# Performance work log

Measured on AMD Instinct MI355X. Metric: run time of the kernel, lower is better.

Reference implementation:

```python
import jax, jax.numpy as jnp
import numpy as np


def setup_inputs() -> dict:
    key = jax.random.key(0)
    k1, k2, k3 = jax.random.split(key, 3)
    # q: [num_seqs, num_heads, head_dim] decode queries (q_len = 1)
    q = jax.random.normal(k1, (32, 32, 128), dtype=jnp.float32)
    # k, v: [sp_shards, num_seqs, kv_len_per_shard, num_kv_heads, head_dim]
    k = jax.random.normal(k2, (4, 32, 1024, 8, 128), dtype=jnp.float32)
    v = jax.random.normal(k3, (4, 32, 1024, 8, 128), dtype=jnp.float32)
    return {"q": q, "k": k, "v": v}


def reference(q, k, v):
    # Flash-decoding style paged decode attention with GQA:
    # each sequence-parallel shard s produces a partial (normalized) output
    # plus per-(seq, head) max logit and exp-sum; gatherlayer then performs
    # the online-softmax merge across shards.
    n, h, d = q.shape
    s, _, L, kv, _ = k.shape
    g = h // kv  # GQA group size
    scale = jnp.asarray(d, q.dtype) ** -0.5
    q4 = q.reshape(n, kv, g, d)

    # --- per-shard partial attention (what self.attn returns per rank) ---
    scores = jnp.einsum('nkgd,snlkd->snkgl', q4, k) * scale  # [s,n,kv,g,L]
    max_logits = scores.max(axis=-1)                          # [s,n,kv,g]
    p = jnp.exp(scores - max_logits[..., None])
    exp_sum = p.sum(axis=-1)                                  # [s,n,kv,g]
    partial = jnp.einsum('snkgl,snlkd->snkgd', p, v) / exp_sum[..., None]

    # --- gatherlayer: online-softmax combine across shards ---
    gmax = max_logits.max(axis=0)                             # [n,kv,g]
    w = jnp.exp(max_logits - gmax) * exp_sum                  # [s,n,kv,g]
    out = (partial * w[..., None]).sum(axis=0) / w.sum(axis=0)[..., None]
    return out.reshape(n, h, d)
```

## Files before the change

kernel.cpp:

```cpp
#include <hip/hip_runtime.h>
#include <math.h>

#define NSEQ 32
#define NH   32
#define NKV  8
#define GRP  4
#define DIM  128
#define NSH  4
#define LSH  1024
#define ITERS 128
#define KVSTRIDE (NKV*DIM)

#define MOFF ((size_t)NSH*NSEQ*NKV*GRP*DIM)
#define SOFF (MOFF + (size_t)NSH*NSEQ*NKV*GRP)

__global__ __launch_bounds__(256, 4) void attn_partial_kernel(
    const float* __restrict__ q, const float* __restrict__ kk,
    const float* __restrict__ vv, float* __restrict__ ws) {
  const int kvh = blockIdx.x;
  const int n   = blockIdx.y;
  const int sh  = blockIdx.z;
  const int tid = threadIdx.x;
  const int w    = tid >> 6;
  const int lane = tid & 63;
  const int sub  = lane & 31;
  const int pgrp = (w << 1) | (lane >> 5);

  const float scale = 0.08838834764831845f;
  const float* qp = q + ((size_t)n * NH + (size_t)kvh * GRP) * DIM + sub * 4;
  float4 qv0 = *(const float4*)(qp + 0 * DIM);
  float4 qv1 = *(const float4*)(qp + 1 * DIM);
  float4 qv2 = *(const float4*)(qp + 2 * DIM);
  float4 qv3 = *(const float4*)(qp + 3 * DIM);
#define SCQ(Q) Q.x *= scale; Q.y *= scale; Q.z *= scale; Q.w *= scale
  SCQ(qv0); SCQ(qv1); SCQ(qv2); SCQ(qv3);
#undef SCQ

  float m0 = -1e30f, m1 = -1e30f, m2 = -1e30f, m3 = -1e30f;
  float s0 = 0.f, s1 = 0.f, s2 = 0.f, s3 = 0.f;
  float4 a0 = make_float4(0.f,0.f,0.f,0.f);
  float4 a1 = a0, a2 = a0, a3 = a0;

  const size_t blkoff = ((size_t)sh * NSEQ + n) * LSH * (size_t)KVSTRIDE
                        + (size_t)kvh * DIM + sub * 4;
  const float* kb = kk + blkoff;
  const float* vb = vv + blkoff;

  auto process = [&](const float4 kc, const float4 vc) {
    float d0 = kc.x*qv0.x + kc.y*qv0.y + kc.z*qv0.z + kc.w*qv0.w;
    float d1 = kc.x*qv1.x + kc.y*qv1.y + kc.z*qv1.z + kc.w*qv1.w;
    float d2 = kc.x*qv2.x + kc.y*qv2.y + kc.z*qv2.z + kc.w*qv2.w;
    float d3 = kc.x*qv3.x + kc.y*qv3.y + kc.z*qv3.z + kc.w*qv3.w;
#pragma unroll
    for (int off = 1; off < 32; off <<= 1) {
      d0 += __shfl_xor(d0, off, 32);
      d1 += __shfl_xor(d1, off, 32);
      d2 += __shfl_xor(d2, off, 32);
      d3 += __shfl_xor(d3, off, 32);
    }
    if (d0 > m0 || d1 > m1 || d2 > m2 || d3 > m3) {
      float nm0 = fmaxf(m0, d0), nm1 = fmaxf(m1, d1);
      float nm2 = fmaxf(m2, d2), nm3 = fmaxf(m3, d3);
      float r0 = __expf(m0 - nm0), r1 = __expf(m1 - nm1);
      float r2 = __expf(m2 - nm2), r3 = __expf(m3 - nm3);
      s0 *= r0; s1 *= r1; s2 *= r2; s3 *= r3;
      a0.x *= r0; a0.y *= r0; a0.z *= r0; a0.w *= r0;
      a1.x *= r1; a1.y *= r1; a1.z *= r1; a1.w *= r1;
      a2.x *= r2; a2.y *= r2; a2.z *= r2; a2.w *= r2;
      a3.x *= r3; a3.y *= r3; a3.z *= r3; a3.w *= r3;
      m0 = nm0; m1 = nm1; m2 = nm2; m3 = nm3;
    }
    float p0 = __expf(d0 - m0), p1 = __expf(d1 - m1);
    float p2 = __expf(d2 - m2), p3 = __expf(d3 - m3);
    s0 += p0; s1 += p1; s2 += p2; s3 += p3;
    a0.x = fmaf(p0, vc.x, a0.x); a0.y = fmaf(p0, vc.y, a0.y);
    a0.z = fmaf(p0, vc.z, a0.z); a0.w = fmaf(p0, vc.w, a0.w);
    a1.x = fmaf(p1, vc.x, a1.x); a1.y = fmaf(p1, vc.y, a1.y);
    a1.z = fmaf(p1, vc.z, a1.z); a1.w = fmaf(p1, vc.w, a1.w);
    a2.x = fmaf(p2, vc.x, a2.x); a2.y = fmaf(p2, vc.y, a2.y);
    a2.z = fmaf(p2, vc.z, a2.z); a2.w = fmaf(p2, vc.w, a2.w);
    a3.x = fmaf(p3, vc.x, a3.x); a3.y = fmaf(p3, vc.y, a3.y);
    a3.z = fmaf(p3, vc.z, a3.z); a3.w = fmaf(p3, vc.w, a3.w);
  };

  float4 k0 = *(const float4*)(kb + (size_t)(0 * 8 + pgrp) * KVSTRIDE);
  float4 v0 = *(const float4*)(vb + (size_t)(0 * 8 + pgrp) * KVSTRIDE);
  float4 k1 = *(const float4*)(kb + (size_t)(1 * 8 + pgrp) * KVSTRIDE);
  float4 v1 = *(const float4*)(vb + (size_t)(1 * 8 + pgrp) * KVSTRIDE);

  for (int it = 0; it < ITERS; it += 2) {
    const int p2i = (it + 2) & (ITERS - 1);
    const int p3i = (it + 3) & (ITERS - 1);
    float4 nk0 = *(const float4*)(kb + (size_t)(p2i * 8 + pgrp) * KVSTRIDE);
    float4 nv0 = *(const float4*)(vb + (size_t)(p2i * 8 + pgrp) * KVSTRIDE);
    float4 nk1 = *(const float4*)(kb + (size_t)(p3i * 8 + pgrp) * KVSTRIDE);
    float4 nv1 = *(const float4*)(vb + (size_t)(p3i * 8 + pgrp) * KVSTRIDE);
    process(k0, v0);
    process(k1, v1);
    k0 = nk0; v0 = nv0; k1 = nk1; v1 = nv1;
  }

#define HALF_MERGE(mX, sX, aX) do {                       \
    float om_ = __shfl_xor(mX, 32, 64);                   \
    float nm_ = fmaxf(mX, om_);                           \
    float ea_ = __expf(mX - nm_), eb_ = __expf(om_ - nm_);\
    float os_ = __shfl_xor(sX, 32, 64);                   \
    sX = sX * ea_ + os_ * eb_;                            \
    float t_;                                             \
    t_ = __shfl_xor(aX.x, 32, 64); aX.x = aX.x*ea_ + t_*eb_; \
    t_ = __shfl_xor(aX.y, 32, 64); aX.y = aX.y*ea_ + t_*eb_; \
    t_ = __shfl_xor(aX.z, 32, 64); aX.z = aX.z*ea_ + t_*eb_; \
    t_ = __shfl_xor(aX.w, 32, 64); aX.w = aX.w*ea_ + t_*eb_; \
    mX = nm_;                                             \
  } while (0)
  HALF_MERGE(m0, s0, a0);
  HALF_MERGE(m1, s1, a1);
  HALF_MERGE(m2, s2, a2);
  HALF_MERGE(m3, s3, a3);
#undef HALF_MERGE

  __shared__ float lm[4][GRP][32];
  __shared__ float lsum[4][GRP][32];
  __shared__ float la[4][GRP][32][4];
  if ((lane >> 5) == 0) {
#define STORE_G(gi, mX, sX, aX)                                   \
    lm[w][gi][sub] = mX; lsum[w][gi][sub] = sX;                   \
    la[w][gi][sub][0] = aX.x; la[w][gi][sub][1] = aX.y;           \
    la[w][gi][sub][2] = aX.z; la[w][gi][sub][3] = aX.w;
    STORE_G(0, m0, s0, a0)
    STORE_G(1, m1, s1, a1)
    STORE_G(2, m2, s2, a2)
    STORE_G(3, m3, s3, a3)
#undef STORE_G
  }
  __syncthreads();

  if (tid < 128) {
    const int gi = tid >> 5;
    const int sb = tid & 31;
    float M = -1e30f, SS = 0.f;
    float A0 = 0.f, A1 = 0.f, A2 = 0.f, A3 = 0.f;
#pragma unroll
    for (int wv = 0; wv < 4; ++wv) {
      float mm = lm[wv][gi][sb];
      float nm = fmaxf(M, mm);
      float ra = __expf(M - nm), rb = __expf(mm - nm);
      SS = SS * ra + lsum[wv][gi][sb] * rb;
      A0 = A0 * ra + la[wv][gi][sb][0] * rb;
      A1 = A1 * ra + la[wv][gi][sb][1] * rb;
      A2 = A2 * ra + la[wv][gi][sb][2] * rb;
      A3 = A3 * ra + la[wv][gi][sb][3] * rb;
      M = nm;
    }
    const size_t idx = (((size_t)sh * NSEQ + n) * NKV + kvh) * GRP + gi;
    *(float4*)(ws + idx * DIM + sb * 4) = make_float4(A0, A1, A2, A3);
    ws[MOFF + idx] = M;
    ws[SOFF + idx] = SS;
  }
}

__global__ __launch_bounds__(128) void attn_merge_kernel(
    const float* __restrict__ ws, float* __restrict__ out) {
  const int kvh = blockIdx.x;
  const int n   = blockIdx.y;
  const int d   = threadIdx.x;
#pragma unroll
  for (int gi = 0; gi < GRP; ++gi) {
    size_t idx[NSH];
    float mm[NSH];
    float M = -1e30f;
#pragma unroll
    for (int s2 = 0; s2 < NSH; ++s2) {
      idx[s2] = (((size_t)s2 * NSEQ + n) * NKV + kvh) * GRP + gi;
      mm[s2] = ws[MOFF + idx[s2]];
      M = fmaxf(M, mm[s2]);
    }
    float num = 0.f, den = 0.f;
#pragma unroll
    for (int s2 = 0; s2 < NSH; ++s2) {
      float wg = __expf(mm[s2] - M);
      den += wg * ws[SOFF + idx[s2]];
      num += wg * ws[idx[s2] * DIM + d];
    }
    out[((size_t)n * NH + (size_t)kvh * GRP + gi) * DIM + d] = num / den;
  }
}

extern "C" void kernel_launch(void* const* d_in, const int* in_sizes, int n_in,
                              void* d_out, int out_size, void* d_ws, size_t ws_size,
                              hipStream_t stream) {
  const float* q = (const float*)d_in[0];
  const float* k = (const float*)d_in[1];
  const float* v = (const float*)d_in[2];
  float* out = (float*)d_out;
  float* ws  = (float*)d_ws;

  attn_partial_kernel<<<dim3(NKV, NSEQ, NSH), 256, 0, stream>>>(q, k, v, ws);
  attn_merge_kernel<<<dim3(NKV, NSEQ), 128, 0, stream>>>(ws, out);
}
```

Before: 185.0 us.

## Fuse cross-shard merge into partial kernel via last-block atomic counter

Removes the separate merge kernel launch. Each partial block increments a per-(kv head, seq) atomic counter, and the last of the four shard blocks to finish performs the online-softmax merge and writes the output. K/V loads now use nontemporal loads, and the prefetch loop drops the wrapped redundant final loads by peeling the last two iterations. In exchange it adds a memset launch for the counters plus threadfence/atomic overhead.

After: 236.9 us. 1.28x slower.

```diff
diff --git a/kernel.cpp b/kernel.cpp
--- a/kernel.cpp
+++ b/kernel.cpp
@@ -13,10 +13,18 @@
 
 #define MOFF ((size_t)NSH*NSEQ*NKV*GRP*DIM)
 #define SOFF (MOFF + (size_t)NSH*NSEQ*NKV*GRP)
-
-__global__ __launch_bounds__(256, 4) void attn_partial_kernel(
+#define CNT_OFF (SOFF + (size_t)NSH*NSEQ*NKV*GRP)
+
+typedef float f32x4_t __attribute__((ext_vector_type(4)));
+__device__ __forceinline__ float4 ntload4(const float* p) {
+  f32x4_t t = __builtin_nontemporal_load(reinterpret_cast<const f32x4_t*>(p));
+  return make_float4(t.x, t.y, t.z, t.w);
+}
+
+__global__ __launch_bounds__(256, 4) void attn_fused_kernel(
     const float* __restrict__ q, const float* __restrict__ kk,
-    const float* __restrict__ vv, float* __restrict__ ws) {
+    const float* __restrict__ vv, float* __restrict__ ws,
+    float* __restrict__ out) {
   const int kvh = blockIdx.x;
   const int n   = blockIdx.y;
   const int sh  = blockIdx.z;
@@ -83,22 +91,24 @@
     a3.z = fmaf(p3, vc.z, a3.z); a3.w = fmaf(p3, vc.w, a3.w);
   };
 
-  float4 k0 = *(const float4*)(kb + (size_t)(0 * 8 + pgrp) * KVSTRIDE);
-  float4 v0 = *(const float4*)(vb + (size_t)(0 * 8 + pgrp) * KVSTRIDE);
-  float4 k1 = *(const float4*)(kb + (size_t)(1 * 8 + pgrp) * KVSTRIDE);
-  float4 v1 = *(const float4*)(vb + (size_t)(1 * 8 + pgrp) * KVSTRIDE);
-
-  for (int it = 0; it < ITERS; it += 2) {
-    const int p2i = (it + 2) & (ITERS - 1);
-    const int p3i = (it + 3) & (ITERS - 1);
-    float4 nk0 = *(const float4*)(kb + (size_t)(p2i * 8 + pgrp) * KVSTRIDE);
-    float4 nv0 = *(const float4*)(vb + (size_t)(p2i * 8 + pgrp) * KVSTRIDE);
-    float4 nk1 = *(const float4*)(kb + (size_t)(p3i * 8 + pgrp) * KVSTRIDE);
-    float4 nv1 = *(const float4*)(vb + (size_t)(p3i * 8 + pgrp) * KVSTRIDE);
+  float4 k0 = ntload4(kb + (size_t)(0 * 8 + pgrp) * KVSTRIDE);
+  float4 v0 = ntload4(vb + (size_t)(0 * 8 + pgrp) * KVSTRIDE);
+  float4 k1 = ntload4(kb + (size_t)(1 * 8 + pgrp) * KVSTRIDE);
+  float4 v1 = ntload4(vb + (size_t)(1 * 8 + pgrp) * KVSTRIDE);
+
+  for (int it = 0; it < ITERS - 2; it += 2) {
+    const int p2i = it + 2;
+    const int p3i = it + 3;
+    float4 nk0 = ntload4(kb + (size_t)(p2i * 8 + pgrp) * KVSTRIDE);
+    float4 nv0 = ntload4(vb + (size_t)(p2i * 8 + pgrp) * KVSTRIDE);
+    float4 nk1 = ntload4(kb + (size_t)(p3i * 8 + pgrp) * KVSTRIDE);
+    float4 nv1 = ntload4(vb + (size_t)(p3i * 8 + pgrp) * KVSTRIDE);
     process(k0, v0);
     process(k1, v1);
     k0 = nk0; v0 = nv0; k1 = nk1; v1 = nv1;
   }
+  process(k0, v0);
+  process(k1, v1);
 
 #define HALF_MERGE(mX, sX, aX) do {                       \
     float om_ = __shfl_xor(mX, 32, 64);                   \
@@ -157,32 +167,41 @@
     ws[MOFF + idx] = M;
     ws[SOFF + idx] = SS;
   }
-}
-
-__global__ __launch_bounds__(128) void attn_merge_kernel(
-    const float* __restrict__ ws, float* __restrict__ out) {
-  const int kvh = blockIdx.x;
-  const int n   = blockIdx.y;
-  const int d   = threadIdx.x;
-#pragma unroll
-  for (int gi = 0; gi < GRP; ++gi) {
-    size_t idx[NSH];
-    float mm[NSH];
-    float M = -1e30f;
-#pragma unroll
-    for (int s2 = 0; s2 < NSH; ++s2) {
-      idx[s2] = (((size_t)s2 * NSEQ + n) * NKV + kvh) * GRP + gi;
-      mm[s2] = ws[MOFF + idx[s2]];
-      M = fmaxf(M, mm[s2]);
-    }
-    float num = 0.f, den = 0.f;
-#pragma unroll
-    for (int s2 = 0; s2 < NSH; ++s2) {
-      float wg = __expf(mm[s2] - M);
-      den += wg * ws[SOFF + idx[s2]];
-      num += wg * ws[idx[s2] * DIM + d];
-    }
-    out[((size_t)n * NH + (size_t)kvh * GRP + gi) * DIM + d] = num / den;
+
+  __syncthreads();
+  __shared__ int is_last;
+  if (tid == 0) {
+    __threadfence();
+    int* cnt = (int*)(ws + CNT_OFF);
+    int prev = atomicAdd(&cnt[kvh * NSEQ + n], 1);
+    is_last = (prev == NSH - 1);
+  }
+  __syncthreads();
+  if (!is_last) return;
+  __threadfence();
+
+  if (tid < 128) {
+    const int d = tid;
+#pragma unroll
+    for (int gi = 0; gi < GRP; ++gi) {
+      size_t idx[NSH];
+      float mm[NSH];
+      float M = -1e30f;
+#pragma unroll
+      for (int s2 = 0; s2 < NSH; ++s2) {
+        idx[s2] = (((size_t)s2 * NSEQ + n) * NKV + kvh) * GRP + gi;
+        mm[s2] = ws[MOFF + idx[s2]];
+        M = fmaxf(M, mm[s2]);
+      }
+      float num = 0.f, den = 0.f;
+#pragma unroll
+      for (int s2 = 0; s2 < NSH; ++s2) {
+        float wg = __expf(mm[s2] - M);
+        den += wg * ws[SOFF + idx[s2]];
+        num += wg * ws[idx[s2] * DIM + d];
+      }
+      out[((size_t)n * NH + (size_t)kvh * GRP + gi) * DIM + d] = num / den;
+    }
   }
 }
 
@@ -195,6 +214,6 @@
   float* out = (float*)d_out;
   float* ws  = (float*)d_ws;
 
-  attn_partial_kernel<<<dim3(NKV, NSEQ, NSH), 256, 0, stream>>>(q, k, v, ws);
-  attn_merge_kernel<<<dim3(NKV, NSEQ), 128, 0, stream>>>(ws, out);
+  hipMemsetAsync(ws + CNT_OFF, 0, NKV * NSEQ * sizeof(int), stream);
+  attn_fused_kernel<<<dim3(NKV, NSEQ, NSH), 256, 0, stream>>>(q, k, v, ws, out);
 }
```
